# Kernel tuning notes

Hardware: AMD Instinct MI355X
Metric: run time of the kernel (lower is better)

## Reference

```python
import jax, jax.numpy as jnp
import numpy as np

B, N, D = 32, 181, 512          # batch, num_projs (seq len), embed_dim
H, HD = 8, 64                   # heads, head_dim
DEPTH, FFN = 6, 2048            # layers, mlp_ratio*embed_dim
MAXLEN = 181                    # RPE max_len (EncoderLayer default)
LN_EPS = 1e-5


def setup_inputs() -> dict:
    key = jax.random.key(0)
    ks = jax.random.split(key, 16)
    rn = lambda k, s, sc=0.02: (jax.random.normal(k, s, jnp.float32) * sc)
    return {
        "x_0": jax.random.normal(ks[0], (B, N, D), jnp.float32),
        "max_shift": 50,
        "pos_embed": rn(ks[1], (1, N, D)),
        "qkv_w": rn(ks[2], (DEPTH, D, 3 * D)), "qkv_b": jnp.zeros((DEPTH, 3 * D), jnp.float32),
        "out_w": rn(ks[3], (DEPTH, D, D)), "out_b": jnp.zeros((DEPTH, D), jnp.float32),
        "rel_pos": jax.random.normal(ks[4], (DEPTH, 2 * MAXLEN - 1, HD), jnp.float32),
        "rpe_w": rn(ks[5], (DEPTH, HD, 1)),
        "ln1_g": jnp.ones((DEPTH, D), jnp.float32), "ln1_b": jnp.zeros((DEPTH, D), jnp.float32),
        "ffn_w1": rn(ks[6], (DEPTH, D, FFN)), "ffn_b1": jnp.zeros((DEPTH, FFN), jnp.float32),
        "ffn_w2": rn(ks[7], (DEPTH, FFN, D)), "ffn_b2": jnp.zeros((DEPTH, D), jnp.float32),
        "ln2_g": jnp.ones((DEPTH, D), jnp.float32), "ln2_b": jnp.zeros((DEPTH, D), jnp.float32),
        "mlp_w1": rn(ks[8], (D, 64)), "mlp_b1": jnp.zeros((64,), jnp.float32),
        "mlp_w2": rn(ks[9], (64, 1)), "mlp_b2": jnp.zeros((1,), jnp.float32),
    }


def _layer_norm(x, g, b):
    m = jnp.mean(x, -1, keepdims=True)
    v = jnp.mean((x - m) ** 2, -1, keepdims=True)
    return (x - m) * jax.lax.rsqrt(v + LN_EPS) * g + b


def reference(x_0, max_shift, pos_embed, qkv_w, qkv_b, out_w, out_b, rel_pos, rpe_w,
              ln1_g, ln1_b, ffn_w1, ffn_b1, ffn_w2, ffn_b2, ln2_g, ln2_b,
              mlp_w1, mlp_b1, mlp_w2, mlp_b2):
    Bb, T, L = x_0.shape
    n_head = H
    hd = L // n_head
    scale = hd ** -0.5
    max_len = (rel_pos.shape[1] + 1) // 2
    # relative position index table [T, T]
    idx = jnp.arange(T)[None, :] - jnp.arange(T)[:, None] + (max_len - 1)

    x = x_0 + pos_embed
    depth = qkv_w.shape[0]
    for i in range(depth):
        # --- MHA with relative position bias ---
        qkv = (x @ qkv_w[i] + qkv_b[i]).reshape(Bb, T, 3, n_head, hd)
        q, k, v = qkv[:, :, 0], qkv[:, :, 1], qkv[:, :, 2]   # [B,T,H,hd]
        scores = jnp.einsum('bqhd,bkhd->bhqk', q, k) * scale
        bias = (rel_pos[i][idx] @ rpe_w[i])[..., 0]          # [T,T]
        scores = scores + bias[None, None]
        w = jax.nn.softmax(scores, axis=-1)
        attn = jnp.einsum('bhqk,bkhd->bqhd', w, v).reshape(Bb, T, L)
        attn = attn @ out_w[i] + out_b[i]
        x = _layer_norm(x + attn, ln1_g[i], ln1_b[i])
        # --- FFN ---
        h = jax.nn.gelu(x @ ffn_w1[i] + ffn_b1[i], approximate=False)
        h = h @ ffn_w2[i] + ffn_b2[i]
        x = _layer_norm(x + h, ln2_g[i], ln2_b[i])

    # per-projection shift head
    shift = jax.nn.relu(x @ mlp_w1 + mlp_b1) @ mlp_w2 + mlp_b2   # [B,T,1]

    # --- SpatialTransformer: bilinear warp along L only (flow[:,0] == 0) ---
    grid_y = 2.0 * (jnp.arange(T, dtype=jnp.float32) / (T - 1) - 0.5)   # [T]
    grid_x = 2.0 * (jnp.arange(L, dtype=jnp.float32) / (L - 1) - 0.5)   # [L]
    flow_x = shift * max_shift / (L // 2)                               # [B,T,1]
    gx = grid_x[None, None, :] + flow_x                                 # [B,T,L]
    # unnormalize (align_corners=False), border padding -> clamp coords
    ix = jnp.clip(((gx + 1.0) * L - 1.0) / 2.0, 0.0, L - 1.0)
    iy = jnp.clip(((grid_y + 1.0) * T - 1.0) / 2.0, 0.0, T - 1.0)       # [T]
    ix0f = jnp.floor(ix); wx = ix - ix0f
    iy0f = jnp.floor(iy); wy = iy - iy0f
    ix0 = jnp.clip(ix0f.astype(jnp.int32), 0, L - 1)
    ix1 = jnp.clip(ix0 + 1, 0, L - 1)
    iy0 = jnp.clip(iy0f.astype(jnp.int32), 0, T - 1)
    iy1 = jnp.clip(iy0 + 1, 0, T - 1)
    bidx = jnp.arange(Bb)[:, None, None]
    iy0b, iy1b = iy0[None, :, None], iy1[None, :, None]
    v00 = x_0[bidx, iy0b, ix0]; v01 = x_0[bidx, iy0b, ix1]
    v10 = x_0[bidx, iy1b, ix0]; v11 = x_0[bidx, iy1b, ix1]
    wyb = wy[None, :, None]
    warped = (1 - wyb) * ((1 - wx) * v00 + wx * v01) + wyb * ((1 - wx) * v10 + wx * v11)
    return shift, warped
```

## Files before the change

kernel.cpp:

```cpp
#include <hip/hip_runtime.h>
#include <hip/hip_bf16.h>
#include <math.h>

#define M_ROWS 5792
#define NTOK 181
#define NLAYER 6

typedef __attribute__((ext_vector_type(8))) _Float16 f16x8;
typedef __attribute__((ext_vector_type(4))) float f32x4;
typedef __attribute__((ext_vector_type(16))) float f32x16;

__device__ __forceinline__ ushort f2h(float f) {
    union { _Float16 h; ushort u; } v;
    v.h = (_Float16)f;
    return v.u;
}
__device__ __forceinline__ float h2f(ushort u) {
    union { ushort u; _Float16 h; } v; v.u = u;
    return (float)v.h;
}
__device__ __forceinline__ float gelu_f(float v) {
    return 0.5f * v * (1.0f + erff(v * 0.70710678118654752f));
}
__device__ __forceinline__ void async16(const void* g, void* l) {
    __builtin_amdgcn_global_load_lds((const __attribute__((address_space(1))) void*)g,
                                     (__attribute__((address_space(3))) void*)l, 16, 0, 0);
}

__global__ __launch_bounds__(256) void wt_all(const float* __restrict__ qkvw,
                                              const float* __restrict__ outw,
                                              const float* __restrict__ fw1,
                                              const float* __restrict__ fw2,
                                              const float* __restrict__ mw1,
                                              const float* __restrict__ relp,
                                              const float* __restrict__ rpew,
                                              ushort* __restrict__ qkv_wt, ushort* __restrict__ out_wt,
                                              ushort* __restrict__ f1_wt, ushort* __restrict__ f2_wt,
                                              ushort* __restrict__ w1t, float* __restrict__ rbias) {
    int id = blockIdx.x;
    if (id >= 4616) {
        id -= 4616;
        const int l = id >> 1;
        const int j = (id & 1) * 256 + threadIdx.x;
        if (j >= 2 * NTOK - 1) return;
        const float* rp = relp + ((size_t)l * (2 * NTOK - 1) + j) * 64;
        const float* wv = rpew + l * 64;
        float s = 0.f;
        #pragma unroll
        for (int d = 0; d < 64; d += 4) {
            float4 a = *(const float4*)(rp + d);
            float4 b = *(const float4*)(wv + d);
            s += a.x*b.x + a.y*b.y + a.z*b.z + a.w*b.w;
        }
        rbias[l * 512 + j] = s;
        return;
    }
    const float* W; ushort* Wt; int K, N;
    if (id < 1152)      { W = qkvw; Wt = qkv_wt; K = 512;  N = 1536; }
    else if (id < 1536) { W = outw; Wt = out_wt; K = 512;  N = 512;  id -= 1152; }
    else if (id < 3072) { W = fw1;  Wt = f1_wt;  K = 512;  N = 2048; id -= 1536; }
    else if (id < 4608) { W = fw2;  Wt = f2_wt;  K = 2048; N = 512;  id -= 3072; }
    else                { W = mw1;  Wt = w1t;    K = 512;  N = 64;   id -= 4608; }
    const int nk = K >> 6, nn = N >> 6;
    const int per = nk * nn;
    const int z = id / per; id -= z * per;
    const int k0 = (id % nk) * 64, n0 = (id / nk) * 64;

    __shared__ float t[64][65];
    const size_t ls = (size_t)z * K * N;
    const float* Wl = W + ls;
    ushort* Wtl = Wt + ls;
    const int tr = threadIdx.x >> 6, tc = threadIdx.x & 63;
    #pragma unroll
    for (int i = 0; i < 16; ++i) {
        const int r = i * 4 + tr;
        t[r][tc] = Wl[(size_t)(k0 + r) * N + n0 + tc];
    }
    __syncthreads();
    #pragma unroll
    for (int i = 0; i < 16; ++i) {
        const int r = i * 4 + tr;
        Wtl[(size_t)(n0 + r) * K + k0 + tc] = f2h(t[tc][r]);
    }
}

__global__ void add_pos_kernel(const float* __restrict__ x0, const float* __restrict__ pos,
                               float* __restrict__ x, ushort* __restrict__ xb) {
    int idx = blockIdx.x * 256 + threadIdx.x;
    const int total = M_ROWS * 128;
    if (idx >= total) return;
    int col = idx & 127;
    int m   = idx >> 7;
    int t   = m % NTOK;
    float4 a = ((const float4*)x0)[idx];
    float4 p = ((const float4*)pos)[t * 128 + col];
    a.x += p.x; a.y += p.y; a.z += p.z; a.w += p.w;
    ((float4*)x)[idx] = a;
    ((ushort4*)xb)[idx] = make_ushort4(f2h(a.x), f2h(a.y), f2h(a.z), f2h(a.w));
}

template<int BM, int EPI, int SK>
__global__ __launch_bounds__(256) void mfma_gemm(const ushort* __restrict__ A,
                                                 const ushort* __restrict__ Bt,
                                                 const float* __restrict__ bias,
                                                 void* __restrict__ Cv,
                                                 int M, int K, int N) {
    constexpr int MREP = BM / 32;
    __shared__ __align__(16) ushort sA[2][BM * 32];
    __shared__ __align__(16) ushort sB[2][128 * 32];

    const int NC  = N >> 7;
    const int NR  = (M + BM - 1) / BM;
    const int NRP = (NR + 7) & ~7;
    const int PSB = NRP * NC;
    const int gid = blockIdx.x;
    const int sk  = (SK > 1) ? gid / PSB : 0;
    const int j   = (SK > 1) ? gid % PSB : gid;
    const int r   = (j / (8 * NC)) * 8 + (j & 7);
    const int c   = (j % (8 * NC)) >> 3;
    if (r >= NR) return;

    const int tid = threadIdx.x;
    const int lane = tid & 63;
    const int w = tid >> 6;
    const int wr = w >> 1, wc = w & 1;
    const int row0 = r * BM, col0 = c * 128;
    const int wbase = tid & ~63;

    f32x4 acc[MREP][4];
    const f32x4 zero = {0.f, 0.f, 0.f, 0.f};
    #pragma unroll
    for (int m = 0; m < MREP; ++m)
        #pragma unroll
        for (int n = 0; n < 4; ++n) acc[m][n] = zero;

    auto stage = [&](int buf, int kt) {
        const int k0 = kt << 5;
        #pragma unroll
        for (int i = 0; i < BM / 64; ++i) {
            const int s = i * 256 + tid;
            const int row = s >> 2;
            const int kbl = (s & 3) ^ ((row >> 1) & 3);
            int gr = row0 + row; if (gr > M - 1) gr = M - 1;
            async16(A + (size_t)gr * K + k0 + (kbl << 3),
                    &sA[buf][(i * 256 + wbase) * 8]);
        }
        #pragma unroll
        for (int i = 0; i < 2; ++i) {
            const int s = i * 256 + tid;
            const int nr = s >> 2;
            const int kbl = (s & 3) ^ ((nr >> 1) & 3);
            async16(Bt + (size_t)(col0 + nr) * K + k0 + (kbl << 3),
                    &sB[buf][(i * 256 + wbase) * 8]);
        }
    };

    const int NIT = (K / SK) >> 5;
    const int kt0 = sk * NIT;
    stage(0, kt0);
    const int l15 = lane & 15, kb = lane >> 4;
    for (int it = 0; it < NIT; ++it) {
        __syncthreads();
        if (it + 1 < NIT) stage((it + 1) & 1, kt0 + it + 1);
        const int buf = it & 1;
        f16x8 af[MREP], bfr[4];
        #pragma unroll
        for (int m = 0; m < MREP; ++m) {
            const int rr = wr * (BM / 2) + m * 16 + l15;
            af[m] = *(const f16x8*)&sA[buf][rr * 32 + ((kb ^ ((rr >> 1) & 3)) << 3)];
        }
        #pragma unroll
        for (int n = 0; n < 4; ++n) {
            const int rr = wc * 64 + n * 16 + l15;
            bfr[n] = *(const f16x8*)&sB[buf][rr * 32 + ((kb ^ ((rr >> 1) & 3)) << 3)];
        }
        #pragma unroll
        for (int m = 0; m < MREP; ++m)
            #pragma unroll
            for (int n = 0; n < 4; ++n)
                acc[m][n] = __builtin_amdgcn_mfma_f32_16x16x32_f16(af[m], bfr[n], acc[m][n], 0, 0, 0);
    }

    const int crow = row0 + wr * (BM / 2) + (lane >> 4) * 4;
    const int ccol = col0 + wc * 64 + l15;
    ushort* outh = (ushort*)Cv + (size_t)sk * M * N;
    #pragma unroll
    for (int m = 0; m < MREP; ++m)
        #pragma unroll
        for (int n = 0; n < 4; ++n) {
            const int gc = ccol + n * 16;
            const float bv = (SK == 1 || sk == 0) ? bias[gc] : 0.f;
            #pragma unroll
            for (int rr = 0; rr < 4; ++rr) {
                const int gr = crow + m * 16 + rr;
                if (gr < M) {
                    float v = acc[m][n][rr] + bv;
                    if (EPI == 1)      outh[(size_t)gr * N + gc] = f2h(gelu_f(v));
                    else if (EPI == 2) outh[(size_t)gr * N + gc] = f2h(v);
                    else               ((float*)Cv)[(size_t)gr * N + gc] = v;
                }
            }
        }
}

__global__ __launch_bounds__(256) void head_mfma(const ushort* __restrict__ A,
                                                 const ushort* __restrict__ Bt,
                                                 const float* __restrict__ b1,
                                                 const float* __restrict__ w2,
                                                 const float* __restrict__ b2,
                                                 float* __restrict__ shift) {
    const int M = M_ROWS, K = 512;
    __shared__ __align__(16) ushort sA[2][128 * 32];
    __shared__ __align__(16) ushort sB[2][64 * 32];
    const int tid = threadIdx.x;
    const int lane = tid & 63;
    const int w = tid >> 6;
    const int row0 = blockIdx.x * 128;
    const int wbase = tid & ~63;

    f32x4 acc[2][4];
    const f32x4 zero = {0.f, 0.f, 0.f, 0.f};
    #pragma unroll
    for (int m = 0; m < 2; ++m)
        #pragma unroll
        for (int n = 0; n < 4; ++n) acc[m][n] = zero;

    auto stage = [&](int buf, int kt) {
        const int k0 = kt << 5;
        #pragma unroll
        for (int i = 0; i < 2; ++i) {
            const int s = i * 256 + tid;
            const int row = s >> 2;
            const int kbl = (s & 3) ^ ((row >> 1) & 3);
            int gr = row0 + row; if (gr > M - 1) gr = M - 1;
            async16(A + (size_t)gr * K + k0 + (kbl << 3),
                    &sA[buf][(i * 256 + wbase) * 8]);
        }
        {
            const int s = tid;
            const int nr = s >> 2;
            const int kbl = (s & 3) ^ ((nr >> 1) & 3);
            async16(Bt + (size_t)nr * K + k0 + (kbl << 3),
                    &sB[buf][wbase * 8]);
        }
    };

    stage(0, 0);
    const int l15 = lane & 15, kb = lane >> 4;
    for (int it = 0; it < 16; ++it) {
        __syncthreads();
        if (it + 1 < 16) stage((it + 1) & 1, it + 1);
        const int buf = it & 1;
        f16x8 af[2], bfr[4];
        #pragma unroll
        for (int m = 0; m < 2; ++m) {
            const int r = w * 32 + m * 16 + l15;
            af[m] = *(const f16x8*)&sA[buf][r * 32 + ((kb ^ ((r >> 1) & 3)) << 3)];
        }
        #pragma unroll
        for (int n = 0; n < 4; ++n) {
            const int r = n * 16 + l15;
            bfr[n] = *(const f16x8*)&sB[buf][r * 32 + ((kb ^ ((r >> 1) & 3)) << 3)];
        }
        #pragma unroll
        for (int m = 0; m < 2; ++m)
            #pragma unroll
            for (int n = 0; n < 4; ++n)
                acc[m][n] = __builtin_amdgcn_mfma_f32_16x16x32_f16(af[m], bfr[n], acc[m][n], 0, 0, 0);
    }

    const float b2v = b2[0];
    float b1v[4], w2v[4];
    #pragma unroll
    for (int n = 0; n < 4; ++n) {
        const int c = n * 16 + l15;
        b1v[n] = b1[c];
        w2v[n] = w2[c];
    }
    #pragma unroll
    for (int m = 0; m < 2; ++m) {
        #pragma unroll
        for (int r = 0; r < 4; ++r) {
            float p = 0.f;
            #pragma unroll
            for (int n = 0; n < 4; ++n)
                p += fmaxf(acc[m][n][r] + b1v[n], 0.f) * w2v[n];
            #pragma unroll
            for (int off = 1; off < 16; off <<= 1) p += __shfl_xor(p, off);
            const int gr = row0 + w * 32 + m * 16 + kb * 4 + r;
            if (l15 == 0 && gr < M) shift[gr] = p + b2v;
        }
    }
}

__global__ __launch_bounds__(384, 1) void attn_fused(const ushort* __restrict__ xb,
                                                     const ushort* __restrict__ Wt,
                                                     const float* __restrict__ bias,
                                                     const float* __restrict__ rb,
                                                     ushort* __restrict__ outb) {
    extern __shared__ __align__(16) char smem[];
    ushort* Ks = (ushort*)smem;
    ushort* Qs = Ks + 12288;
    ushort* vt = Qs + 12288;
    ushort* sA = vt + 12288;
    ushort* sB = sA + 12288;
    float*  rs = (float*)(smem + 122880);

    const int b = blockIdx.x >> 3;
    const int h = blockIdx.x & 7;
    const int tid = threadIdx.x, lane = tid & 63, w = tid >> 6;
    const int l31 = lane & 31, hi = lane >> 5;
    const int l15 = lane & 15, kb = lane >> 4;
    const int wbase = tid & ~63;

    for (int i = tid; i < 416; i += 384) {
        int j = i - 32;
        rs[i] = (j >= 0 && j < 2 * NTOK - 1) ? rb[j] : 0.f;
    }

    const ushort* Arow = xb + (size_t)(b * NTOK) * 512;

    auto stage = [&](int buf, int it) {
        const int k0 = it << 5;
        #pragma unroll
        for (int i = 0; i < 2; ++i) {
            const int s = i * 384 + tid;
            const int row = s >> 2;
            const int kbl = (s & 3) ^ ((row >> 1) & 3);
            const int gr = row < NTOK ? row : NTOK - 1;
            async16(Arow + (size_t)gr * 512 + k0 + (kbl << 3),
                    &sA[buf * 6144 + (i * 384 + wbase) * 8]);
        }
        #pragma unroll
        for (int i = 0; i < 2; ++i) {
            const int s = i * 384 + tid;
            const int n = s >> 2;
            const int kbl = (s & 3) ^ ((n >> 1) & 3);
            const int wrow = (n >> 6) * 512 + h * 64 + (n & 63);
            async16(Wt + (size_t)wrow * 512 + k0 + (kbl << 3),
                    &sB[buf * 6144 + (i * 384 + wbase) * 8]);
        }
    };

    f32x4 acc[24];
    const f32x4 zero = {0.f, 0.f, 0.f, 0.f};
    #pragma unroll
    for (int t = 0; t < 24; ++t) acc[t] = zero;

    const int cb = (w < 4) ? ((w >> 1) * 64 + (w & 1) * 32)
                           : (128 + (w - 4) * 32);

    stage(0, 0);
    for (int it = 0; it < 16; ++it) {
        __syncthreads();
        if (it + 1 < 16) stage((it + 1) & 1, it + 1);
        const ushort* a  = &sA[(it & 1) * 6144];
        const ushort* bw = &sB[(it & 1) * 6144];
        if (w < 4) {
            f16x8 af[12], bf[2];
            #pragma unroll
            for (int mt = 0; mt < 12; ++mt) {
                const int r = mt * 16 + l15;
                af[mt] = *(const f16x8*)&a[r * 32 + ((kb ^ ((r >> 1) & 3)) << 3)];
            }
            #pragma unroll
            for (int nt = 0; nt < 2; ++nt) {
                const int n = cb + nt * 16 + l15;
                bf[nt] = *(const f16x8*)&bw[n * 32 + ((kb ^ ((n >> 1) & 3)) << 3)];
            }
            #pragma unroll
            for (int mt = 0; mt < 12; ++mt)
                #pragma unroll
                for (int nt = 0; nt < 2; ++nt)
                    acc[mt * 2 + nt] = __builtin_amdgcn_mfma_f32_16x16x32_f16(af[mt], bf[nt], acc[mt * 2 + nt], 0, 0, 0);
        } else {
            f16x8 af[2], bf[12];
            #pragma unroll
            for (int mt = 0; mt < 2; ++mt) {
                const int n = cb + mt * 16 + l15;
                af[mt] = *(const f16x8*)&bw[n * 32 + ((kb ^ ((n >> 1) & 3)) << 3)];
            }
            #pragma unroll
            for (int nt = 0; nt < 12; ++nt) {
                const int r = nt * 16 + l15;
                bf[nt] = *(const f16x8*)&a[r * 32 + ((kb ^ ((r >> 1) & 3)) << 3)];
            }
            #pragma unroll
            for (int mt = 0; mt < 2; ++mt)
                #pragma unroll
                for (int nt = 0; nt < 12; ++nt)
                    acc[mt * 12 + nt] = __builtin_amdgcn_mfma_f32_16x16x32_f16(af[mt], bf[nt], acc[mt * 12 + nt], 0, 0, 0);
        }
    }

    if (w < 4) {
        ushort* dst = (w < 2) ? Qs : Ks;
        const int dbase = (w & 1) * 32;
        const int boff = (w < 2 ? 0 : 512) + h * 64;
        #pragma unroll
        for (int nt = 0; nt < 2; ++nt) {
            const int d = dbase + nt * 16 + l15;
            const float bv = bias[boff + d];
            #pragma unroll
            for (int mt = 0; mt < 12; ++mt)
                #pragma unroll
                for (int r = 0; r < 4; ++r) {
                    const int tok = mt * 16 + kb * 4 + r;
                    dst[tok * 64 + (((d >> 3) ^ (tok & 7)) << 3) + (d & 7)] =
                        f2h(acc[mt * 2 + nt][r] + bv);
                }
        }
    } else {
        const int dbase = (w - 4) * 32;
        #pragma unroll
        for (int mt = 0; mt < 2; ++mt)
            #pragma unroll
            for (int r = 0; r < 4; ++r) {
                const int d = dbase + mt * 16 + kb * 4 + r;
                const float bv = bias[1024 + h * 64 + d];
                const int sd = (d ^ (d >> 3)) & 7;
                #pragma unroll
                for (int nt = 0; nt < 12; ++nt) {
                    const int tok = nt * 16 + l15;
                    vt[d * 192 + (((tok >> 3) ^ sd) << 3) + (tok & 7)] =
                        f2h(acc[mt * 12 + nt][r] + bv);
                }
            }
    }
    __syncthreads();

    {
        const int q0 = w * 32;
        const int q = q0 + l31;
        f16x8 qf[4];
        #pragma unroll
        for (int ds = 0; ds < 4; ++ds)
            qf[ds] = *(const f16x8*)&Qs[q * 64 + (((2 * ds + hi) ^ (q & 7)) << 3)];

        f32x16 S[6];
        #pragma unroll
        for (int kt = 0; kt < 6; ++kt)
            #pragma unroll
            for (int r = 0; r < 16; ++r) S[kt][r] = 0.f;
        __builtin_amdgcn_s_setprio(1);
        #pragma unroll
        for (int kt = 0; kt < 6; ++kt) {
            const int krow = kt * 32 + l31;
            #pragma unroll
            for (int ds = 0; ds < 4; ++ds) {
                f16x8 kf = *(const f16x8*)&Ks[krow * 64 + (((2 * ds + hi) ^ (krow & 7)) << 3)];
                S[kt] = __builtin_amdgcn_mfma_f32_32x32x16_f16(kf, qf[ds], S[kt], 0, 0, 0);
            }
        }
        __builtin_amdgcn_s_setprio(0);

        float mx = -1e30f;
        #pragma unroll
        for (int kt = 0; kt < 6; ++kt)
            #pragma unroll
            for (int r = 0; r < 16; ++r) {
                const int k = kt * 32 + (r & 3) + 8 * (r >> 2) + 4 * hi;
                float s = (k < NTOK) ? S[kt][r] * 0.125f + rs[k - q + 212] : -1e30f;
                S[kt][r] = s;
                mx = fmaxf(mx, s);
            }
        mx = fmaxf(mx, __shfl_xor(mx, 32));
        float sum = 0.f;
        #pragma unroll
        for (int kt = 0; kt < 6; ++kt)
            #pragma unroll
            for (int r = 0; r < 16; ++r) {
                float e = __expf(S[kt][r] - mx);
                S[kt][r] = e;
                sum += e;
            }
        sum += __shfl_xor(sum, 32);
        const float inv = 1.0f / sum;
        #pragma unroll
        for (int kt = 0; kt < 6; ++kt)
            #pragma unroll
            for (int r = 0; r < 16; ++r) S[kt][r] *= inv;

        f32x16 O[2];
        #pragma unroll
        for (int nt = 0; nt < 2; ++nt)
            #pragma unroll
            for (int r = 0; r < 16; ++r) O[nt][r] = 0.f;
        #pragma unroll
        for (int kt2 = 0; kt2 < 12; ++kt2) {
            const int kt = kt2 >> 1, half = kt2 & 1;
            uint p[4];
            #pragma unroll
            for (int m = 0; m < 4; ++m)
                p[m] = (uint)f2h(S[kt][8 * half + 2 * m]) |
                       ((uint)f2h(S[kt][8 * half + 2 * m + 1]) << 16);
            const uint s0l = (uint)__shfl_xor((int)p[0], 32);
            const uint s0h = (uint)__shfl_xor((int)p[1], 32);
            const uint s1l = (uint)__shfl_xor((int)p[2], 32);
            const uint s1h = (uint)__shfl_xor((int)p[3], 32);
            uint fa[4];
            if (hi == 0) { fa[0] = p[0]; fa[1] = p[1]; fa[2] = s0l; fa[3] = s0h; }
            else         { fa[0] = s1l; fa[1] = s1h; fa[2] = p[2]; fa[3] = p[3]; }
            const f16x8 pa = *(const f16x8*)fa;
            __builtin_amdgcn_s_setprio(1);
            #pragma unroll
            for (int nt = 0; nt < 2; ++nt) {
                const int d = nt * 32 + l31;
                f16x8 vf = *(const f16x8*)&vt[d * 192 + (((2 * kt2 + hi) ^ ((d ^ (d >> 3)) & 7)) << 3)];
                O[nt] = __builtin_amdgcn_mfma_f32_32x32x16_f16(pa, vf, O[nt], 0, 0, 0);
            }
            __builtin_amdgcn_s_setprio(0);
        }

        #pragma unroll
        for (int nt = 0; nt < 2; ++nt)
            #pragma unroll
            for (int r = 0; r < 16; ++r) {
                const int qr = q0 + (r & 3) + 8 * (r >> 2) + 4 * hi;
                if (qr < NTOK)
                    outb[(size_t)(b * NTOK + qr) * 512 + h * 64 + nt * 32 + l31] = f2h(O[nt][r]);
            }
    }
}

template<int NY>
__global__ __launch_bounds__(256) void lnres_kernel(float* __restrict__ x, ushort* __restrict__ xb,
                                                    const ushort* __restrict__ y,
                                                    const ushort* __restrict__ y1,
                                                    const float* __restrict__ g, const float* __restrict__ bb) {
    const int row = blockIdx.x * 4 + (threadIdx.x >> 6);
    const int l = threadIdx.x & 63;
    float* xr = x + (size_t)row * 512;
    ushort* xbr = xb + (size_t)row * 512;
    const ushort* yr = y + (size_t)row * 512;
    float4 v0 = *(const float4*)(xr + (l << 2));
    float4 v1 = *(const float4*)(xr + 256 + (l << 2));
    const ushort4 u0 = *(const ushort4*)(yr + (l << 2));
    const ushort4 u1 = *(const ushort4*)(yr + 256 + (l << 2));
    v0.x += h2f(u0.x); v0.y += h2f(u0.y); v0.z += h2f(u0.z); v0.w += h2f(u0.w);
    v1.x += h2f(u1.x); v1.y += h2f(u1.y); v1.z += h2f(u1.z); v1.w += h2f(u1.w);
    if (NY == 2) {
        const ushort* y1r = y1 + (size_t)row * 512;
        const ushort4 w0 = *(const ushort4*)(y1r + (l << 2));
        const ushort4 w1 = *(const ushort4*)(y1r + 256 + (l << 2));
        v0.x += h2f(w0.x); v0.y += h2f(w0.y); v0.z += h2f(w0.z); v0.w += h2f(w0.w);
        v1.x += h2f(w1.x); v1.y += h2f(w1.y); v1.z += h2f(w1.z); v1.w += h2f(w1.w);
    }
    float s = v0.x + v0.y + v0.z + v0.w + v1.x + v1.y + v1.z + v1.w;
    #pragma unroll
    for (int off = 32; off; off >>= 1) s += __shfl_xor(s, off);
    const float m = s * (1.0f / 512.0f);
    float d0 = v0.x - m, d1 = v0.y - m, d2 = v0.z - m, d3 = v0.w - m;
    float d4 = v1.x - m, d5 = v1.y - m, d6 = v1.z - m, d7 = v1.w - m;
    float q = d0*d0 + d1*d1 + d2*d2 + d3*d3 + d4*d4 + d5*d5 + d6*d6 + d7*d7;
    #pragma unroll
    for (int off = 32; off; off >>= 1) q += __shfl_xor(q, off);
    const float r = rsqrtf(q * (1.0f / 512.0f) + 1e-5f);
    const float4 g0 = *(const float4*)(g + (l << 2));
    const float4 g1 = *(const float4*)(g + 256 + (l << 2));
    const float4 b0 = *(const float4*)(bb + (l << 2));
    const float4 b1 = *(const float4*)(bb + 256 + (l << 2));
    float4 o0, o1;
    o0.x = d0 * r * g0.x + b0.x; o0.y = d1 * r * g0.y + b0.y;
    o0.z = d2 * r * g0.z + b0.z; o0.w = d3 * r * g0.w + b0.w;
    o1.x = d4 * r * g1.x + b1.x; o1.y = d5 * r * g1.y + b1.y;
    o1.z = d6 * r * g1.z + b1.z; o1.w = d7 * r * g1.w + b1.w;
    *(float4*)(xr + (l << 2)) = o0;
    *(float4*)(xr + 256 + (l << 2)) = o1;
    *(ushort4*)(xbr + (l << 2)) = make_ushort4(f2h(o0.x), f2h(o0.y), f2h(o0.z), f2h(o0.w));
    *(ushort4*)(xbr + 256 + (l << 2)) = make_ushort4(f2h(o1.x), f2h(o1.y), f2h(o1.z), f2h(o1.w));
}

__global__ void warp_kernel(const float* __restrict__ x0, const float* __restrict__ shift,
                            const int* __restrict__ pms, float* __restrict__ warped) {
    int idx = blockIdx.x * 256 + threadIdx.x;
    if (idx >= M_ROWS * 512) return;
    int c = idx & 511;
    int m = idx >> 9;
    int t = m % NTOK;
    int b = m / NTOK;
    float max_shift = (float)pms[0];
    float sh = shift[m];
    float flow = sh * max_shift / 256.0f;
    float gx = 2.0f * ((float)c / 511.0f - 0.5f) + flow;
    float ix = ((gx + 1.0f) * 512.0f - 1.0f) * 0.5f;
    ix = fminf(fmaxf(ix, 0.0f), 511.0f);
    float gy = 2.0f * ((float)t / 180.0f - 0.5f);
    float iy = ((gy + 1.0f) * 181.0f - 1.0f) * 0.5f;
    iy = fminf(fmaxf(iy, 0.0f), 180.0f);
    float ix0f = floorf(ix), iy0f = floorf(iy);
    float wx = ix - ix0f, wy = iy - iy0f;
    int ix0 = min(max((int)ix0f, 0), 511);
    int ix1 = min(ix0 + 1, 511);
    int iy0 = min(max((int)iy0f, 0), 180);
    int iy1 = min(iy0 + 1, 180);
    const float* xb = x0 + (size_t)b * NTOK * 512;
    float v00 = xb[iy0 * 512 + ix0], v01 = xb[iy0 * 512 + ix1];
    float v10 = xb[iy1 * 512 + ix0], v11 = xb[iy1 * 512 + ix1];
    warped[idx] = (1.f - wy) * ((1.f - wx) * v00 + wx * v01) + wy * ((1.f - wx) * v10 + wx * v11);
}

extern "C" void kernel_launch(void* const* d_in, const int* in_sizes, int n_in,
                              void* d_out, int out_size, void* d_ws, size_t ws_size,
                              hipStream_t stream) {
    const float* x0   = (const float*)d_in[0];
    const int*   pms  = (const int*)d_in[1];
    const float* pos  = (const float*)d_in[2];
    const float* qkvw = (const float*)d_in[3];
    const float* qkvb = (const float*)d_in[4];
    const float* outw = (const float*)d_in[5];
    const float* outbp= (const float*)d_in[6];
    const float* relp = (const float*)d_in[7];
    const float* rpew = (const float*)d_in[8];
    const float* ln1g = (const float*)d_in[9];
    const float* ln1b = (const float*)d_in[10];
    const float* fw1  = (const float*)d_in[11];
    const float* fb1  = (const float*)d_in[12];
    const float* fw2  = (const float*)d_in[13];
    const float* fb2  = (const float*)d_in[14];
    const float* ln2g = (const float*)d_in[15];
    const float* ln2b = (const float*)d_in[16];
    const float* mw1  = (const float*)d_in[17];
    const float* mb1  = (const float*)d_in[18];
    const float* mw2  = (const float*)d_in[19];
    const float* mb2  = (const float*)d_in[20];

    float* out = (float*)d_out;

    char* ws = (char*)d_ws;
    float*  x     = (float*)ws;
    ushort* xb    = (ushort*)(ws + 11862016);
    char*   qr    = ws + 11862016 + 5931008;
    ushort* ybuf  = (ushort*)qr;
    ushort* ybuf2 = (ushort*)(qr + 5931008);
    ushort* hbuf  = (ushort*)(qr + 11862016);
    ushort* attnb = (ushort*)(qr + 35586048);
    float*  rbias = (float*)(qr + 35586048 + 5931008);
    ushort* wts   = (ushort*)(qr + 35586048 + 5931008 + 12288);
    ushort* qkv_wt = wts;
    ushort* out_wt = qkv_wt + 6 * 1536 * 512;
    ushort* f1_wt  = out_wt + 6 * 512 * 512;
    ushort* f2_wt  = f1_wt  + 6 * 512 * 2048;
    ushort* w1t    = f2_wt  + 6 * 2048 * 512;

    hipFuncSetAttribute((const void*)attn_fused,
                        hipFuncAttributeMaxDynamicSharedMemorySize, 124544);

    wt_all<<<4628, 256, 0, stream>>>(qkvw, outw, fw1, fw2, mw1, relp, rpew,
                                     qkv_wt, out_wt, f1_wt, f2_wt, w1t, rbias);

    add_pos_kernel<<<(M_ROWS * 128 + 255) / 256, 256, 0, stream>>>(x0, pos, x, xb);

    const int g_ffn1 = 96 * 16;
    const int g_np4  = 96 * 4;
    for (int i = 0; i < NLAYER; ++i) {
        attn_fused<<<256, 384, 124544, stream>>>(xb, qkv_wt + (size_t)i * 1536 * 512,
                                                 qkvb + i * 1536, rbias + i * 512, attnb);
        mfma_gemm<64, 2, 2><<<g_np4 * 2, 256, 0, stream>>>(attnb, out_wt + (size_t)i * 512 * 512,
                                                           outbp + i * 512, ybuf, M_ROWS, 512, 512);
        lnres_kernel<2><<<1448, 256, 0, stream>>>(x, xb, ybuf, ybuf2, ln1g + i * 512, ln1b + i * 512);
        mfma_gemm<64, 1, 1><<<g_ffn1, 256, 0, stream>>>(xb, f1_wt + (size_t)i * 2048 * 512,
                                                        fb1 + i * 2048, hbuf, M_ROWS, 512, 2048);
        mfma_gemm<64, 2, 2><<<g_np4 * 2, 256, 0, stream>>>(hbuf, f2_wt + (size_t)i * 512 * 2048,
                                                           fb2 + i * 512, ybuf, M_ROWS, 2048, 512);
        lnres_kernel<2><<<1448, 256, 0, stream>>>(x, xb, ybuf, ybuf2, ln2g + i * 512, ln2b + i * 512);
    }

    head_mfma<<<46, 256, 0, stream>>>(xb, w1t, mb1, mw2, mb2, out);
    warp_kernel<<<(M_ROWS * 512 + 255) / 256, 256, 0, stream>>>(x0, out, pms, out + M_ROWS);
}
```

Baseline: 679.1 us.

## Drop fp32 residual stream, keep fp16 only; fuse add_pos into weight prep

Removes the fp32 residual copy x. The layernorm-residual kernel now reads the residual from the fp16 activation buffer xb and writes only fp16, which cuts global memory traffic in every lnres launch. The positional-embedding add is folded into the weight-transpose launch as extra blocks, saving one kernel launch. The cost is lower precision: the residual stream is now accumulated in fp16 across all layers, which may raise numerical error.

```diff
diff --git a/kernel.cpp b/kernel.cpp
--- a/kernel.cpp
+++ b/kernel.cpp
@@ -34,10 +34,25 @@
                                               const float* __restrict__ mw1,
                                               const float* __restrict__ relp,
                                               const float* __restrict__ rpew,
+                                              const float* __restrict__ x0,
+                                              const float* __restrict__ pos,
                                               ushort* __restrict__ qkv_wt, ushort* __restrict__ out_wt,
                                               ushort* __restrict__ f1_wt, ushort* __restrict__ f2_wt,
-                                              ushort* __restrict__ w1t, float* __restrict__ rbias) {
+                                              ushort* __restrict__ w1t, float* __restrict__ rbias,
+                                              ushort* __restrict__ xb) {
     int id = blockIdx.x;
+    if (id >= 4628) {
+        const int idx = (id - 4628) * 256 + threadIdx.x;
+        if (idx >= M_ROWS * 128) return;
+        const int col = idx & 127;
+        const int m   = idx >> 7;
+        const int t   = m % NTOK;
+        float4 a = ((const float4*)x0)[idx];
+        float4 p = ((const float4*)pos)[t * 128 + col];
+        a.x += p.x; a.y += p.y; a.z += p.z; a.w += p.w;
+        ((ushort4*)xb)[idx] = make_ushort4(f2h(a.x), f2h(a.y), f2h(a.z), f2h(a.w));
+        return;
+    }
     if (id >= 4616) {
         id -= 4616;
         const int l = id >> 1;
@@ -82,21 +97,6 @@
         const int r = i * 4 + tr;
         Wtl[(size_t)(n0 + r) * K + k0 + tc] = f2h(t[tc][r]);
     }
-}
-
-__global__ void add_pos_kernel(const float* __restrict__ x0, const float* __restrict__ pos,
-                               float* __restrict__ x, ushort* __restrict__ xb) {
-    int idx = blockIdx.x * 256 + threadIdx.x;
-    const int total = M_ROWS * 128;
-    if (idx >= total) return;
-    int col = idx & 127;
-    int m   = idx >> 7;
-    int t   = m % NTOK;
-    float4 a = ((const float4*)x0)[idx];
-    float4 p = ((const float4*)pos)[t * 128 + col];
-    a.x += p.x; a.y += p.y; a.z += p.z; a.w += p.w;
-    ((float4*)x)[idx] = a;
-    ((ushort4*)xb)[idx] = make_ushort4(f2h(a.x), f2h(a.y), f2h(a.z), f2h(a.w));
 }
 
 template<int BM, int EPI, int SK>
@@ -524,21 +524,22 @@
 }
 
 template<int NY>
-__global__ __launch_bounds__(256) void lnres_kernel(float* __restrict__ x, ushort* __restrict__ xb,
+__global__ __launch_bounds__(256) void lnres_kernel(ushort* __restrict__ xb,
                                                     const ushort* __restrict__ y,
                                                     const ushort* __restrict__ y1,
                                                     const float* __restrict__ g, const float* __restrict__ bb) {
     const int row = blockIdx.x * 4 + (threadIdx.x >> 6);
     const int l = threadIdx.x & 63;
-    float* xr = x + (size_t)row * 512;
     ushort* xbr = xb + (size_t)row * 512;
     const ushort* yr = y + (size_t)row * 512;
-    float4 v0 = *(const float4*)(xr + (l << 2));
-    float4 v1 = *(const float4*)(xr + 256 + (l << 2));
+    const ushort4 a0 = *(const ushort4*)(xbr + (l << 2));
+    const ushort4 a1 = *(const ushort4*)(xbr + 256 + (l << 2));
     const ushort4 u0 = *(const ushort4*)(yr + (l << 2));
     const ushort4 u1 = *(const ushort4*)(yr + 256 + (l << 2));
-    v0.x += h2f(u0.x); v0.y += h2f(u0.y); v0.z += h2f(u0.z); v0.w += h2f(u0.w);
-    v1.x += h2f(u1.x); v1.y += h2f(u1.y); v1.z += h2f(u1.z); v1.w += h2f(u1.w);
+    float4 v0 = make_float4(h2f(a0.x) + h2f(u0.x), h2f(a0.y) + h2f(u0.y),
+                            h2f(a0.z) + h2f(u0.z), h2f(a0.w) + h2f(u0.w));
+    float4 v1 = make_float4(h2f(a1.x) + h2f(u1.x), h2f(a1.y) + h2f(u1.y),
+                            h2f(a1.z) + h2f(u1.z), h2f(a1.w) + h2f(u1.w));
     if (NY == 2) {
         const ushort* y1r = y1 + (size_t)row * 512;
         const ushort4 w0 = *(const ushort4*)(y1r + (l << 2));
@@ -565,8 +566,6 @@
     o0.z = d2 * r * g0.z + b0.z; o0.w = d3 * r * g0.w + b0.w;
     o1.x = d4 * r * g1.x + b1.x; o1.y = d5 * r * g1.y + b1.y;
     o1.z = d6 * r * g1.z + b1.z; o1.w = d7 * r * g1.w + b1.w;
-    *(float4*)(xr + (l << 2)) = o0;
-    *(float4*)(xr + 256 + (l << 2)) = o1;
     *(ushort4*)(xbr + (l << 2)) = make_ushort4(f2h(o0.x), f2h(o0.y), f2h(o0.z), f2h(o0.w));
     *(ushort4*)(xbr + 256 + (l << 2)) = make_ushort4(f2h(o1.x), f2h(o1.y), f2h(o1.z), f2h(o1.w));
 }
@@ -628,7 +627,6 @@
     float* out = (float*)d_out;
 
     char* ws = (char*)d_ws;
-    float*  x     = (float*)ws;
     ushort* xb    = (ushort*)(ws + 11862016);
     char*   qr    = ws + 11862016 + 5931008;
     ushort* ybuf  = (ushort*)qr;
@@ -646,10 +644,8 @@
     hipFuncSetAttribute((const void*)attn_fused,
                         hipFuncAttributeMaxDynamicSharedMemorySize, 124544);
 
-    wt_all<<<4628, 256, 0, stream>>>(qkvw, outw, fw1, fw2, mw1, relp, rpew,
-                                     qkv_wt, out_wt, f1_wt, f2_wt, w1t, rbias);
-
-    add_pos_kernel<<<(M_ROWS * 128 + 255) / 256, 256, 0, stream>>>(x0, pos, x, xb);
+    wt_all<<<7524, 256, 0, stream>>>(qkvw, outw, fw1, fw2, mw1, relp, rpew, x0, pos,
+                                     qkv_wt, out_wt, f1_wt, f2_wt, w1t, rbias, xb);
 
     const int g_ffn1 = 96 * 16;
     const int g_np4  = 96 * 4;
@@ -658,12 +654,12 @@
                                                  qkvb + i * 1536, rbias + i * 512, attnb);
         mfma_gemm<64, 2, 2><<<g_np4 * 2, 256, 0, stream>>>(attnb, out_wt + (size_t)i * 512 * 512,
                                                            outbp + i * 512, ybuf, M_ROWS, 512, 512);
-        lnres_kernel<2><<<1448, 256, 0, stream>>>(x, xb, ybuf, ybuf2, ln1g + i * 512, ln1b + i * 512);
+        lnres_kernel<2><<<1448, 256, 0, stream>>>(xb, ybuf, ybuf2, ln1g + i * 512, ln1b + i * 512);
         mfma_gemm<64, 1, 1><<<g_ffn1, 256, 0, stream>>>(xb, f1_wt + (size_t)i * 2048 * 512,
                                                         fb1 + i * 2048, hbuf, M_ROWS, 512, 2048);
         mfma_gemm<64, 2, 2><<<g_np4 * 2, 256, 0, stream>>>(hbuf, f2_wt + (size_t)i * 512 * 2048,
                                                            fb2 + i * 512, ybuf, M_ROWS, 2048, 512);
-        lnres_kernel<2><<<1448, 256, 0, stream>>>(x, xb, ybuf, ybuf2, ln2g + i * 512, ln2b + i * 512);
+        lnres_kernel<2><<<1448, 256, 0, stream>>>(xb, ybuf, ybuf2, ln2g + i * 512, ln2b + i * 512);
     }
 
     head_mfma<<<46, 256, 0, stream>>>(xb, w1t, mb1, mw2, mb2, out);
```

Result: faster. 650.1 us (-4.3%).
